# Kernel tuning notes

Hardware: AMD Instinct MI355X
Metric: run time of the kernel (lower is better)

The kernel has to match this reference:

```python
import jax, jax.numpy as jnp
import numpy as np

KLD_SCALE = 10.0
COMMITMENT_COST = 0.25


def setup_inputs() -> dict:
    key = jax.random.key(0)
    k1, k2 = jax.random.split(key)
    B, N, D, K = 8192, 32, 64, 1024
    z = jax.random.normal(k1, (B, N, D), dtype=jnp.float32)
    embed_w = jax.random.normal(k2, (K, N * D), dtype=jnp.float32)
    return {"z": z, "embed_w": embed_w}


def reference(z, embed_w):
    B, N, D = z.shape
    zf = z.reshape(B, N * D)  # b (n d)
    # squared L2 distance to each codebook vector via GEMM expansion
    dist = (jnp.sum(zf * zf, axis=1, keepdims=True)
            - 2.0 * zf @ embed_w.T
            + jnp.sum(embed_w * embed_w, axis=1)[None, :])  # [B, K]
    ind = jnp.argmin(dist, axis=1)  # [B]
    z_q = embed_w[ind]  # [B, N*D] gather
    latent_loss = (COMMITMENT_COST * jnp.mean((jax.lax.stop_gradient(z_q) - zf) ** 2)
                   + jnp.mean((z_q - jax.lax.stop_gradient(zf)) ** 2))
    latent_loss = latent_loss * KLD_SCALE
    z_q = zf + jax.lax.stop_gradient(z_q - zf)  # straight-through
    return z_q, latent_loss
```

## Files before the change

### kernel.cpp

```cpp
#include <hip/hip_runtime.h>

#define NB 8192
#define NK 1024
#define ND 2048
#define DELTA 4.0f

typedef __bf16 bf16x8 __attribute__((ext_vector_type(8)));
typedef float f32x4 __attribute__((ext_vector_type(4)));

static __device__ __forceinline__ unsigned short f2bf(float f) {
    unsigned u = __float_as_uint(f);
    unsigned r = (u + 0x7fff + ((u >> 16) & 1)) >> 16;
    return (unsigned short)r;
}

static __device__ __forceinline__ void async16(const void* g, void* l) {
    __builtin_amdgcn_global_load_lds(
        (const __attribute__((address_space(1))) void*)g,
        (__attribute__((address_space(3))) void*)l, 16, 0, 0);
}

static __device__ __forceinline__ unsigned skey(float s) {
    unsigned u = __float_as_uint(s);
    return (s >= 0.f) ? (u | 0x80000000u) : ~u;
}

static __device__ __forceinline__ void conv_row(const float* __restrict__ src,
                                                unsigned short* __restrict__ dst,
                                                float* __restrict__ nrm, int l) {
    const float4* row = (const float4*)src;
    ushort4* orow = (ushort4*)dst;
    float s = 0.f;
#pragma unroll
    for (int i = 0; i < 8; ++i) {
        float4 v = row[l + 64 * i];
        s += v.x * v.x + v.y * v.y + v.z * v.z + v.w * v.w;
        ushort4 h;
        h.x = f2bf(v.x); h.y = f2bf(v.y); h.z = f2bf(v.z); h.w = f2bf(v.w);
        orow[l + 64 * i] = h;
    }
#pragma unroll
    for (int m = 32; m; m >>= 1) s += __shfl_xor(s, m, 64);
    if (l == 0) *nrm = s;
}

__global__ __launch_bounds__(256)
void prep_kernel(const float* __restrict__ z, const float* __restrict__ e,
                 unsigned short* __restrict__ zh, unsigned short* __restrict__ eh,
                 float* __restrict__ znorm, float* __restrict__ enorm) {
    const int w = threadIdx.x >> 6, l = threadIdx.x & 63;
    if (blockIdx.x < NB / 4) {
        const int b = blockIdx.x * 4 + w;
        conv_row(z + (size_t)b * ND, zh + (size_t)b * ND, znorm + b, l);
    } else {
        const int k = (blockIdx.x - NB / 4) * 4 + w;
        conv_row(e + (size_t)k * ND, eh + (size_t)k * ND, enorm + k, l);
    }
}

__global__ __launch_bounds__(256)
void coarse_gemm_kernel(const unsigned short* __restrict__ zh,
                        const unsigned short* __restrict__ eh,
                        const float* __restrict__ enorm,
                        float* __restrict__ pmin, ulonglong2* __restrict__ pmask) {
    __shared__ __align__(16) unsigned short As[128 * 64];
    __shared__ __align__(16) unsigned short Bs[128 * 64];
    __shared__ float rmin[128][2];
    __shared__ unsigned long long rmask[128][2];

    const int t = threadIdx.x;
    const int w = t >> 6, l = t & 63;
    const int wr = w & 1, wc = w >> 1;
    const int rowBase = blockIdx.x * 128;
    const int colBase = blockIdx.y * 128;

    f32x4 acc[4][4];
#pragma unroll
    for (int m = 0; m < 4; ++m)
#pragma unroll
        for (int n = 0; n < 4; ++n) acc[m][n] = (f32x4)(0.0f);

    const int r0  = t >> 3;
    const int csw = (t & 7) ^ (r0 & 7);
    const size_t zsrc = (size_t)(rowBase + r0) * ND + csw * 8;
    const size_t esrc = (size_t)(colBase + r0) * ND + csw * 8;

    for (int k0 = 0; k0 < ND; k0 += 64) {
#pragma unroll
        for (int i = 0; i < 4; ++i) {
            async16(zh + zsrc + (size_t)i * 32 * ND + k0, &As[i * 2048 + w * 512]);
            async16(eh + esrc + (size_t)i * 32 * ND + k0, &Bs[i * 2048 + w * 512]);
        }
        __syncthreads();
#pragma unroll
        for (int kk = 0; kk < 2; ++kk) {
            bf16x8 af[4], bfr[4];
#pragma unroll
            for (int m = 0; m < 4; ++m) {
                int r = wr * 64 + m * 16 + (l & 15);
                int ch = ((l >> 4) + kk * 4) ^ (l & 7);
                af[m] = *(const bf16x8*)&As[r * 64 + ch * 8];
            }
#pragma unroll
            for (int n = 0; n < 4; ++n) {
                int r = wc * 64 + n * 16 + (l & 15);
                int ch = ((l >> 4) + kk * 4) ^ (l & 7);
                bfr[n] = *(const bf16x8*)&Bs[r * 64 + ch * 8];
            }
#pragma unroll
            for (int m = 0; m < 4; ++m)
#pragma unroll
                for (int n = 0; n < 4; ++n)
                    acc[m][n] = __builtin_amdgcn_mfma_f32_16x16x32_bf16(af[m], bfr[n], acc[m][n], 0, 0, 0);
        }
        __syncthreads();
    }

    float en[4];
#pragma unroll
    for (int n = 0; n < 4; ++n)
        en[n] = enorm[colBase + wc * 64 + n * 16 + (l & 15)];
    const int g = l >> 4;

#pragma unroll
    for (int m = 0; m < 4; ++m) {
#pragma unroll
        for (int j = 0; j < 4; ++j) {
            float mn = 3.0e38f;
#pragma unroll
            for (int n = 0; n < 4; ++n)
                mn = fminf(mn, en[n] - 2.0f * acc[m][n][j]);
#pragma unroll
            for (int d = 1; d < 16; d <<= 1) mn = fminf(mn, __shfl_xor(mn, d, 64));
            if ((l & 15) == 0) rmin[wr * 64 + m * 16 + g * 4 + j][wc] = mn;
        }
    }
    __syncthreads();

#pragma unroll
    for (int m = 0; m < 4; ++m) {
#pragma unroll
        for (int j = 0; j < 4; ++j) {
            int rl = wr * 64 + m * 16 + g * 4 + j;
            float thr = fminf(rmin[rl][0], rmin[rl][1]) + DELTA;
            unsigned long long seg = 0;
#pragma unroll
            for (int n = 0; n < 4; ++n) {
                unsigned long long bal = __ballot((en[n] - 2.0f * acc[m][n][j]) <= thr);
                seg |= ((bal >> (16 * g)) & 0xFFFFull) << (n * 16);
            }
            if ((l & 15) == 0) rmask[rl][wc] = seg;
        }
    }
    __syncthreads();
    if (t < 128) {
        size_t idx = (size_t)(rowBase + t) * 8 + blockIdx.y;
        pmin[idx] = fminf(rmin[t][0], rmin[t][1]);
        ulonglong2 mk; mk.x = rmask[t][0]; mk.y = rmask[t][1];
        pmask[idx] = mk;
    }
}

__global__ __launch_bounds__(256)
void tail_kernel(const float* __restrict__ pmin, const ulonglong2* __restrict__ pmask,
                 const float* __restrict__ z, const float* __restrict__ e,
                 const float* __restrict__ enorm, const float* __restrict__ znorm,
                 float* __restrict__ out, float* __restrict__ loss) {
    __shared__ float red[4];
    const int w = threadIdx.x >> 6, l = threadIdx.x & 63;
    const int b = blockIdx.x * 4 + w;

    float v = pmin[(size_t)b * 8 + (l & 7)];
#pragma unroll
    for (int d = 1; d < 8; d <<= 1) v = fminf(v, __shfl_xor(v, d, 64));
    const float thr = v + DELTA;

    unsigned long long mlo = 0, mhi = 0;
    int cnt = 0, kc = -1;
    if (l < 8) {
        float pc = pmin[(size_t)b * 8 + l];
        if (pc <= thr) {
            ulonglong2 mk = pmask[(size_t)b * 8 + l];
            mlo = mk.x; mhi = mk.y;
            cnt = __popcll(mlo) + __popcll(mhi);
            if (cnt) kc = l * 128 + (mlo ? (__ffsll((long long)mlo) - 1)
                                         : 64 + (__ffsll((long long)mhi) - 1));
        }
    }
    int tot = cnt;
#pragma unroll
    for (int d = 1; d < 8; d <<= 1) {
        tot += __shfl_xor(tot, d, 64);
        kc = max(kc, __shfl_xor(kc, d, 64));
    }
    tot = __shfl(tot, 0, 64);
    kc  = __shfl(kc, 0, 64);

    int bestk;
    float srow;
    if (tot == 1) {
        bestk = kc;
        srow  = v;
    } else {
        float bestv = 3.0e38f; bestk = 0x7fffffff;
        const float4* z4 = (const float4*)(z + (size_t)b * ND);
        for (int c = 0; c < 8; ++c) {
            unsigned long long lo = __shfl(mlo, c, 64);
            unsigned long long hi = __shfl(mhi, c, 64);
            while (lo | hi) {
                int k;
                if (lo) { int bit = __ffsll((long long)lo) - 1; lo &= lo - 1; k = c * 128 + bit; }
                else    { int bit = __ffsll((long long)hi) - 1; hi &= hi - 1; k = c * 128 + 64 + bit; }
                const float4* e4 = (const float4*)(e + (size_t)k * ND);
                float dot = 0.f;
#pragma unroll
                for (int q = 0; q < 8; ++q) {
                    float4 a = z4[l + 64 * q], bb = e4[l + 64 * q];
                    dot += a.x * bb.x + a.y * bb.y + a.z * bb.z + a.w * bb.w;
                }
#pragma unroll
                for (int d2 = 32; d2; d2 >>= 1) dot += __shfl_xor(dot, d2, 64);
                float s = enorm[k] - 2.0f * dot;
                if (s < bestv) { bestv = s; bestk = k; }
            }
        }
        srow = bestv;
    }

    const float4* q4 = (const float4*)(e + (size_t)bestk * ND);
    float4* o4 = (float4*)(out + (size_t)b * ND);
#pragma unroll
    for (int i = 0; i < 8; ++i) o4[l + 64 * i] = q4[l + 64 * i];

    if (l == 0) red[w] = znorm[b] + srow;
    __syncthreads();
    if (threadIdx.x == 0) {
        float s = (red[0] + red[1]) + (red[2] + red[3]);
        atomicAdd(loss, s * (12.5f / 16777216.0f));
    }
}

#define BK 16
#define LDS_STRIDE 20

__global__ void enorm_kernel(const float* __restrict__ e, float* __restrict__ enorm) {
    const int k = blockIdx.x;
    const int lane = threadIdx.x;
    const float4* row = (const float4*)(e + (size_t)k * ND);
    float s = 0.f;
#pragma unroll
    for (int i = 0; i < 8; ++i) {
        float4 v = row[lane + 64 * i];
        s += v.x * v.x + v.y * v.y + v.z * v.z + v.w * v.w;
    }
#pragma unroll
    for (int m = 32; m; m >>= 1) s += __shfl_xor(s, m, 64);
    if (lane == 0) enorm[k] = s;
}

__global__ __launch_bounds__(256, 2)
void argmin_kernel(const float* __restrict__ z, const float* __restrict__ e,
                   const float* __restrict__ enorm,
                   float* __restrict__ pminv, int* __restrict__ pmini) {
    __shared__ float zs[128 * LDS_STRIDE];
    __shared__ float es[128 * LDS_STRIDE];
    const int t  = threadIdx.x;
    const int tx = t & 31;
    const int ty = t >> 5;
    const int rowBase = blockIdx.x * 128;
    const int colBase = blockIdx.y * 128;

    float acc[16][4];
#pragma unroll
    for (int i = 0; i < 16; ++i)
#pragma unroll
        for (int j = 0; j < 4; ++j) acc[i][j] = 0.f;

    const int srow = t >> 2;
    const int sc4  = t & 3;

    for (int k0 = 0; k0 < ND; k0 += BK) {
#pragma unroll
        for (int q = 0; q < 2; ++q) {
            int r = srow + 64 * q;
            float4 vz = *(const float4*)(z + (size_t)(rowBase + r) * ND + k0 + sc4 * 4);
            *(float4*)(zs + r * LDS_STRIDE + sc4 * 4) = vz;
            float4 ve = *(const float4*)(e + (size_t)(colBase + r) * ND + k0 + sc4 * 4);
            *(float4*)(es + r * LDS_STRIDE + sc4 * 4) = ve;
        }
        __syncthreads();
#pragma unroll
        for (int g = 0; g < BK / 4; ++g) {
            float4 ef[4];
#pragma unroll
            for (int j = 0; j < 4; ++j)
                ef[j] = *(const float4*)(es + (tx + 32 * j) * LDS_STRIDE + g * 4);
#pragma unroll
            for (int i = 0; i < 16; ++i) {
                float4 zf = *(const float4*)(zs + (ty + 8 * i) * LDS_STRIDE + g * 4);
#pragma unroll
                for (int j = 0; j < 4; ++j) {
                    acc[i][j] += zf.x * ef[j].x;
                    acc[i][j] += zf.y * ef[j].y;
                    acc[i][j] += zf.z * ef[j].z;
                    acc[i][j] += zf.w * ef[j].w;
                }
            }
        }
        __syncthreads();
    }
#pragma unroll
    for (int i = 0; i < 16; ++i) {
        float bv = 3.0e38f; int bi = 0x7fffffff;
#pragma unroll
        for (int j = 0; j < 4; ++j) {
            int cg = colBase + tx + 32 * j;
            float s = enorm[cg] - 2.0f * acc[i][j];
            if (s < bv) { bv = s; bi = cg; }
        }
#pragma unroll
        for (int m = 16; m; m >>= 1) {
            float ov = __shfl_xor(bv, m, 64);
            int   oi = __shfl_xor(bi, m, 64);
            if (ov < bv || (ov == bv && oi < bi)) { bv = ov; bi = oi; }
        }
        if (tx == 0) {
            int r = rowBase + ty + 8 * i;
            pminv[(size_t)r * 8 + blockIdx.y] = bv;
            pmini[(size_t)r * 8 + blockIdx.y] = bi;
        }
    }
}

__global__ void final_argmin_kernel(const float* __restrict__ pminv,
                                    const int* __restrict__ pmini,
                                    int* __restrict__ ind) {
    int b = blockIdx.x * 256 + threadIdx.x;
    if (b >= NB) return;
    float bv = pminv[(size_t)b * 8];
    int   bi = pmini[(size_t)b * 8];
#pragma unroll
    for (int c = 1; c < 8; ++c) {
        float v  = pminv[(size_t)b * 8 + c];
        int   i2 = pmini[(size_t)b * 8 + c];
        if (v < bv || (v == bv && i2 < bi)) { bv = v; bi = i2; }
    }
    ind[b] = bi;
}

__global__ __launch_bounds__(256)
void gather_loss_kernel(const float* __restrict__ z, const float* __restrict__ e,
                        const int* __restrict__ ind, float* __restrict__ out,
                        float* __restrict__ loss) {
    const int NT4 = NB * ND / 4;
    float accm = 0.f;
    for (int f = blockIdx.x * blockDim.x + threadIdx.x; f < NT4;
         f += gridDim.x * blockDim.x) {
        int b  = f >> 9;
        int k4 = f & 511;
        const float4 q  = *(const float4*)(e + (size_t)ind[b] * ND + (size_t)k4 * 4);
        const float4 zz = *(const float4*)(z + (size_t)f * 4);
        *(float4*)(out + (size_t)f * 4) = q;
        float dx = q.x - zz.x, dy = q.y - zz.y, dz = q.z - zz.z, dw = q.w - zz.w;
        accm += dx * dx + dy * dy + dz * dz + dw * dw;
    }
#pragma unroll
    for (int m = 32; m; m >>= 1) accm += __shfl_xor(accm, m, 64);
    __shared__ float red[4];
    int lane = threadIdx.x & 63, w = threadIdx.x >> 6;
    if (lane == 0) red[w] = accm;
    __syncthreads();
    if (threadIdx.x == 0) {
        float s = (red[0] + red[1]) + (red[2] + red[3]);
        atomicAdd(loss, s * (12.5f / 16777216.0f));
    }
}

extern "C" void kernel_launch(void* const* d_in, const int* in_sizes, int n_in,
                              void* d_out, int out_size, void* d_ws, size_t ws_size,
                              hipStream_t stream) {
    const float* z = (const float*)d_in[0];
    const float* e = (const float*)d_in[1];
    float* out  = (float*)d_out;
    float* loss = out + (size_t)NB * ND;
    char* W = (char*)d_ws;

    const size_t OFF_ZH    = 0;
    const size_t OFF_EH    = 33554432;
    const size_t OFF_PMIN  = 37748736;
    const size_t OFF_PMASK = 38010880;
    const size_t OFF_EN    = 39059456;
    const size_t OFF_ZN    = 39063552;
    const size_t NEED_FAST = 39096320 + 4096;

    hipMemsetAsync(loss, 0, sizeof(float), stream);

    if (ws_size >= NEED_FAST) {
        unsigned short* zh = (unsigned short*)(W + OFF_ZH);
        unsigned short* eh = (unsigned short*)(W + OFF_EH);
        float* pmin        = (float*)(W + OFF_PMIN);
        ulonglong2* pmask  = (ulonglong2*)(W + OFF_PMASK);
        float* enorm       = (float*)(W + OFF_EN);
        float* znorm       = (float*)(W + OFF_ZN);

        hipLaunchKernelGGL(prep_kernel, dim3(NB / 4 + NK / 4), dim3(256), 0, stream,
                           z, e, zh, eh, znorm, enorm);
        hipLaunchKernelGGL(coarse_gemm_kernel, dim3(NB / 128, NK / 128), dim3(256), 0, stream,
                           zh, eh, enorm, pmin, pmask);
        hipLaunchKernelGGL(tail_kernel, dim3(NB / 4), dim3(256), 0, stream,
                           pmin, pmask, z, e, enorm, znorm, out, loss);
    } else {
        float* enorm = (float*)W;
        float* pminv = (float*)(W + 4096);
        int*   pmini = (int*)(W + 4096 + 262144);
        int*   ind   = (int*)(W + 4096 + 524288);

        hipLaunchKernelGGL(enorm_kernel, dim3(NK), dim3(64), 0, stream, e, enorm);
        hipLaunchKernelGGL(argmin_kernel, dim3(NB / 128, NK / 128), dim3(256), 0, stream,
                           z, e, enorm, pminv, pmini);
        hipLaunchKernelGGL(final_argmin_kernel, dim3(NB / 256), dim3(256), 0, stream,
                           pminv, pmini, ind);
        hipLaunchKernelGGL(gather_loss_kernel, dim3(2048), dim3(256), 0, stream,
                           z, e, ind, out, loss);
    }
}
```

Baseline: 98.47 us.

## Use 128x256 GEMM tiles with triple-buffered async pipeline and split tail kernels

The coarse GEMM grows to 512-thread blocks covering 128x256 output tiles. Operand loads are triple-buffered through LDS with explicit vmcnt waits and raw barriers, and MFMA issue is bracketed with setprio so prefetch overlaps compute. The tail kernel is split into a resolve kernel that writes packed (score, index) keys, a single-block loss reduction that replaces the memset and atomics, and a grid-stride gather kernel. The intent is to cut redundant operand loads and hide memory latency, at the cost of two extra kernel launches and a serial single-block loss pass.

```diff
diff --git a/kernel.cpp b/kernel.cpp
--- a/kernel.cpp
+++ b/kernel.cpp
@@ -7,6 +7,10 @@
 
 typedef __bf16 bf16x8 __attribute__((ext_vector_type(8)));
 typedef float f32x4 __attribute__((ext_vector_type(4)));
+
+#define FENCE asm volatile("" ::: "memory")
+#define WAIT_VM6 asm volatile("s_waitcnt vmcnt(6)" ::: "memory")
+#define WAIT_VM0 asm volatile("s_waitcnt vmcnt(0)" ::: "memory")
 
 static __device__ __forceinline__ unsigned short f2bf(float f) {
     unsigned u = __float_as_uint(f);
@@ -58,21 +62,21 @@
     }
 }
 
-__global__ __launch_bounds__(256)
-void coarse_gemm_kernel(const unsigned short* __restrict__ zh,
-                        const unsigned short* __restrict__ eh,
-                        const float* __restrict__ enorm,
-                        float* __restrict__ pmin, ulonglong2* __restrict__ pmask) {
-    __shared__ __align__(16) unsigned short As[128 * 64];
-    __shared__ __align__(16) unsigned short Bs[128 * 64];
-    __shared__ float rmin[128][2];
-    __shared__ unsigned long long rmask[128][2];
+__global__ __launch_bounds__(512, 1)
+void gemm8_kernel(const unsigned short* __restrict__ zh,
+                  const unsigned short* __restrict__ eh,
+                  const float* __restrict__ enorm,
+                  float* __restrict__ pmin, ulonglong2* __restrict__ pmask) {
+    __shared__ __align__(16) unsigned short S[3 * 24576];
+    __shared__ float rmin[128][4];
+    __shared__ unsigned long long rmask[128][4];
 
     const int t = threadIdx.x;
     const int w = t >> 6, l = t & 63;
-    const int wr = w & 1, wc = w >> 1;
+    const int wr = w >> 2, wc = w & 3;
+    const int lr = l & 15, lg = l >> 4, lx = l & 7;
     const int rowBase = blockIdx.x * 128;
-    const int colBase = blockIdx.y * 128;
+    const int colBase = blockIdx.y * 256;
 
     f32x4 acc[4][4];
 #pragma unroll
@@ -80,47 +84,86 @@
 #pragma unroll
         for (int n = 0; n < 4; ++n) acc[m][n] = (f32x4)(0.0f);
 
-    const int r0  = t >> 3;
-    const int csw = (t & 7) ^ (r0 & 7);
-    const size_t zsrc = (size_t)(rowBase + r0) * ND + csw * 8;
-    const size_t esrc = (size_t)(colBase + r0) * ND + csw * 8;
-
-    for (int k0 = 0; k0 < ND; k0 += 64) {
-#pragma unroll
-        for (int i = 0; i < 4; ++i) {
-            async16(zh + zsrc + (size_t)i * 32 * ND + k0, &As[i * 2048 + w * 512]);
-            async16(eh + esrc + (size_t)i * 32 * ND + k0, &Bs[i * 2048 + w * 512]);
-        }
-        __syncthreads();
-#pragma unroll
-        for (int kk = 0; kk < 2; ++kk) {
-            bf16x8 af[4], bfr[4];
-#pragma unroll
-            for (int m = 0; m < 4; ++m) {
-                int r = wr * 64 + m * 16 + (l & 15);
-                int ch = ((l >> 4) + kk * 4) ^ (l & 7);
-                af[m] = *(const bf16x8*)&As[r * 64 + ch * 8];
-            }
-#pragma unroll
-            for (int n = 0; n < 4; ++n) {
-                int r = wc * 64 + n * 16 + (l & 15);
-                int ch = ((l >> 4) + kk * 4) ^ (l & 7);
-                bfr[n] = *(const bf16x8*)&Bs[r * 64 + ch * 8];
-            }
-#pragma unroll
-            for (int m = 0; m < 4; ++m)
-#pragma unroll
-                for (int n = 0; n < 4; ++n)
-                    acc[m][n] = __builtin_amdgcn_mfma_f32_16x16x32_bf16(af[m], bfr[n], acc[m][n], 0, 0, 0);
-        }
-        __syncthreads();
-    }
+    const int r = t >> 3;
+    const int csw = (t & 7) ^ (r & 7);
+    const unsigned short* zsrc = zh + (size_t)(rowBase + r) * ND + csw * 8;
+    const unsigned short* esrc = eh + (size_t)(colBase + r) * ND + csw * 8;
+    const int wofs = w * 512;
+
+#define STAGE_H0(K0, SL) do { \
+        async16(zsrc + (K0),           &S[(SL) * 24576 +         wofs]); \
+        async16(zsrc + 64 * ND + (K0), &S[(SL) * 24576 +  4096 + wofs]); \
+        async16(esrc + (K0),           &S[(SL) * 24576 +  8192 + wofs]); } while (0)
+#define STAGE_H1(K0, SL) do { \
+        async16(esrc +  64 * ND + (K0), &S[(SL) * 24576 + 12288 + wofs]); \
+        async16(esrc + 128 * ND + (K0), &S[(SL) * 24576 + 16384 + wofs]); \
+        async16(esrc + 192 * ND + (K0), &S[(SL) * 24576 + 20480 + wofs]); } while (0)
+
+    STAGE_H0(0, 0);  STAGE_H1(0, 0);
+    STAGE_H0(64, 1); STAGE_H1(64, 1);
+    WAIT_VM6; FENCE; __builtin_amdgcn_s_barrier(); FENCE;
+
+    int scur = 0;
+    for (int tau = 0; tau < 32; ++tau) {
+        const unsigned short* SA = &S[scur * 24576];
+        const unsigned short* SB = SA + 8192;
+        const int spre = (scur == 0) ? 2 : scur - 1;
+        const int kpre = (tau + 2) * 64;
+
+        if (tau < 30) STAGE_H0(kpre, spre);
+        bf16x8 bfr[4][2], af[2][2];
+#pragma unroll
+        for (int n = 0; n < 4; ++n)
+#pragma unroll
+            for (int kk = 0; kk < 2; ++kk)
+                bfr[n][kk] = *(const bf16x8*)&SB[(wc * 64 + n * 16 + lr) * 64
+                                                 + (((lg + kk * 4) ^ lx) * 8)];
+#pragma unroll
+        for (int mm = 0; mm < 2; ++mm)
+#pragma unroll
+            for (int kk = 0; kk < 2; ++kk)
+                af[mm][kk] = *(const bf16x8*)&SA[(wr * 64 + mm * 16 + lr) * 64
+                                                 + (((lg + kk * 4) ^ lx) * 8)];
+        __builtin_amdgcn_s_setprio(1);
+#pragma unroll
+        for (int mm = 0; mm < 2; ++mm)
+#pragma unroll
+            for (int n = 0; n < 4; ++n)
+#pragma unroll
+                for (int kk = 0; kk < 2; ++kk)
+                    acc[mm][n] = __builtin_amdgcn_mfma_f32_16x16x32_bf16(
+                        af[mm][kk], bfr[n][kk], acc[mm][n], 0, 0, 0);
+        __builtin_amdgcn_s_setprio(0);
+
+        if (tau < 30) STAGE_H1(kpre, spre);
+#pragma unroll
+        for (int mm = 0; mm < 2; ++mm)
+#pragma unroll
+            for (int kk = 0; kk < 2; ++kk)
+                af[mm][kk] = *(const bf16x8*)&SA[(wr * 64 + (mm + 2) * 16 + lr) * 64
+                                                 + (((lg + kk * 4) ^ lx) * 8)];
+        __builtin_amdgcn_s_setprio(1);
+#pragma unroll
+        for (int mm = 0; mm < 2; ++mm)
+#pragma unroll
+            for (int n = 0; n < 4; ++n)
+#pragma unroll
+                for (int kk = 0; kk < 2; ++kk)
+                    acc[mm + 2][n] = __builtin_amdgcn_mfma_f32_16x16x32_bf16(
+                        af[mm][kk], bfr[n][kk], acc[mm + 2][n], 0, 0, 0);
+        __builtin_amdgcn_s_setprio(0);
+
+        if (tau < 30) { WAIT_VM6; } else { WAIT_VM0; }
+        FENCE; __builtin_amdgcn_s_barrier(); FENCE;
+        scur = (scur == 2) ? 0 : scur + 1;
+    }
+#undef STAGE_H0
+#undef STAGE_H1
 
     float en[4];
 #pragma unroll
     for (int n = 0; n < 4; ++n)
-        en[n] = enorm[colBase + wc * 64 + n * 16 + (l & 15)];
-    const int g = l >> 4;
+        en[n] = enorm[colBase + wc * 64 + n * 16 + lr];
 
 #pragma unroll
     for (int m = 0; m < 4; ++m) {
@@ -132,7 +175,7 @@
                 mn = fminf(mn, en[n] - 2.0f * acc[m][n][j]);
 #pragma unroll
             for (int d = 1; d < 16; d <<= 1) mn = fminf(mn, __shfl_xor(mn, d, 64));
-            if ((l & 15) == 0) rmin[wr * 64 + m * 16 + g * 4 + j][wc] = mn;
+            if (lr == 0) rmin[wr * 64 + m * 16 + lg * 4 + j][wc] = mn;
         }
     }
     __syncthreads();
@@ -141,32 +184,36 @@
     for (int m = 0; m < 4; ++m) {
 #pragma unroll
         for (int j = 0; j < 4; ++j) {
-            int rl = wr * 64 + m * 16 + g * 4 + j;
-            float thr = fminf(rmin[rl][0], rmin[rl][1]) + DELTA;
+            int rl = wr * 64 + m * 16 + lg * 4 + j;
+            float thr = fminf(fminf(rmin[rl][0], rmin[rl][1]),
+                              fminf(rmin[rl][2], rmin[rl][3])) + DELTA;
             unsigned long long seg = 0;
 #pragma unroll
             for (int n = 0; n < 4; ++n) {
                 unsigned long long bal = __ballot((en[n] - 2.0f * acc[m][n][j]) <= thr);
-                seg |= ((bal >> (16 * g)) & 0xFFFFull) << (n * 16);
+                seg |= ((bal >> (16 * lg)) & 0xFFFFull) << (n * 16);
             }
-            if ((l & 15) == 0) rmask[rl][wc] = seg;
+            if (lr == 0) rmask[rl][wc] = seg;
         }
     }
     __syncthreads();
+
     if (t < 128) {
-        size_t idx = (size_t)(rowBase + t) * 8 + blockIdx.y;
-        pmin[idx] = fminf(rmin[t][0], rmin[t][1]);
-        ulonglong2 mk; mk.x = rmask[t][0]; mk.y = rmask[t][1];
-        pmask[idx] = mk;
+        float m4 = fminf(fminf(rmin[t][0], rmin[t][1]), fminf(rmin[t][2], rmin[t][3]));
+        size_t idx = (size_t)(rowBase + t) * 8 + (size_t)blockIdx.y * 2;
+        pmin[idx] = m4;
+        ulonglong2 mk0; mk0.x = rmask[t][0]; mk0.y = rmask[t][1];
+        pmask[idx] = mk0;
+        pmin[idx + 1] = m4;
+        ulonglong2 mk1; mk1.x = rmask[t][2]; mk1.y = rmask[t][3];
+        pmask[idx + 1] = mk1;
     }
 }
 
 __global__ __launch_bounds__(256)
-void tail_kernel(const float* __restrict__ pmin, const ulonglong2* __restrict__ pmask,
-                 const float* __restrict__ z, const float* __restrict__ e,
-                 const float* __restrict__ enorm, const float* __restrict__ znorm,
-                 float* __restrict__ out, float* __restrict__ loss) {
-    __shared__ float red[4];
+void resolve2_kernel(const float* __restrict__ pmin, const ulonglong2* __restrict__ pmask,
+                     const float* __restrict__ z, const float* __restrict__ e,
+                     const float* __restrict__ enorm, unsigned long long* __restrict__ best) {
     const int w = threadIdx.x >> 6, l = threadIdx.x & 63;
     const int b = blockIdx.x * 4 + w;
 
@@ -196,47 +243,65 @@
     tot = __shfl(tot, 0, 64);
     kc  = __shfl(kc, 0, 64);
 
-    int bestk;
-    float srow;
     if (tot == 1) {
-        bestk = kc;
-        srow  = v;
-    } else {
-        float bestv = 3.0e38f; bestk = 0x7fffffff;
-        const float4* z4 = (const float4*)(z + (size_t)b * ND);
-        for (int c = 0; c < 8; ++c) {
-            unsigned long long lo = __shfl(mlo, c, 64);
-            unsigned long long hi = __shfl(mhi, c, 64);
-            while (lo | hi) {
-                int k;
-                if (lo) { int bit = __ffsll((long long)lo) - 1; lo &= lo - 1; k = c * 128 + bit; }
-                else    { int bit = __ffsll((long long)hi) - 1; hi &= hi - 1; k = c * 128 + 64 + bit; }
-                const float4* e4 = (const float4*)(e + (size_t)k * ND);
-                float dot = 0.f;
-#pragma unroll
-                for (int q = 0; q < 8; ++q) {
-                    float4 a = z4[l + 64 * q], bb = e4[l + 64 * q];
-                    dot += a.x * bb.x + a.y * bb.y + a.z * bb.z + a.w * bb.w;
-                }
-#pragma unroll
-                for (int d2 = 32; d2; d2 >>= 1) dot += __shfl_xor(dot, d2, 64);
-                float s = enorm[k] - 2.0f * dot;
-                if (s < bestv) { bestv = s; bestk = k; }
+        if (l == 0) best[b] = ((unsigned long long)skey(v) << 32) | (unsigned)kc;
+        return;
+    }
+
+    float bestv = 3.0e38f; int bestk = 0x7fffffff;
+    const float4* z4 = (const float4*)(z + (size_t)b * ND);
+    for (int c = 0; c < 8; ++c) {
+        unsigned long long lo = __shfl(mlo, c, 64);
+        unsigned long long hi = __shfl(mhi, c, 64);
+        while (lo | hi) {
+            int k;
+            if (lo) { int bit = __ffsll((long long)lo) - 1; lo &= lo - 1; k = c * 128 + bit; }
+            else    { int bit = __ffsll((long long)hi) - 1; hi &= hi - 1; k = c * 128 + 64 + bit; }
+            const float4* e4 = (const float4*)(e + (size_t)k * ND);
+            float dot = 0.f;
+#pragma unroll
+            for (int q = 0; q < 8; ++q) {
+                float4 a = z4[l + 64 * q], bb = e4[l + 64 * q];
+                dot += a.x * bb.x + a.y * bb.y + a.z * bb.z + a.w * bb.w;
             }
-        }
-        srow = bestv;
-    }
-
-    const float4* q4 = (const float4*)(e + (size_t)bestk * ND);
-    float4* o4 = (float4*)(out + (size_t)b * ND);
-#pragma unroll
-    for (int i = 0; i < 8; ++i) o4[l + 64 * i] = q4[l + 64 * i];
-
-    if (l == 0) red[w] = znorm[b] + srow;
+#pragma unroll
+            for (int d2 = 32; d2; d2 >>= 1) dot += __shfl_xor(dot, d2, 64);
+            float s = enorm[k] - 2.0f * dot;
+            if (s < bestv) { bestv = s; bestk = k; }
+        }
+    }
+    if (l == 0) best[b] = ((unsigned long long)skey(bestv) << 32) | (unsigned)bestk;
+}
+
+__global__ __launch_bounds__(256)
+void loss1_kernel(const unsigned long long* __restrict__ best,
+                  const float* __restrict__ znorm, float* __restrict__ loss) {
+    float s = 0.f;
+    for (int b = threadIdx.x; b < NB; b += 256) {
+        unsigned key = (unsigned)(best[b] >> 32);
+        unsigned ub = (key & 0x80000000u) ? (key ^ 0x80000000u) : ~key;
+        s += znorm[b] + __uint_as_float(ub);
+    }
+#pragma unroll
+    for (int m = 32; m; m >>= 1) s += __shfl_xor(s, m, 64);
+    __shared__ float red[4];
+    int lane = threadIdx.x & 63, w = threadIdx.x >> 6;
+    if (lane == 0) red[w] = s;
     __syncthreads();
-    if (threadIdx.x == 0) {
-        float s = (red[0] + red[1]) + (red[2] + red[3]);
-        atomicAdd(loss, s * (12.5f / 16777216.0f));
+    if (threadIdx.x == 0)
+        loss[0] = ((red[0] + red[1]) + (red[2] + red[3])) * (12.5f / 16777216.0f);
+}
+
+__global__ __launch_bounds__(256)
+void gather_kernel(const float* __restrict__ e, const unsigned long long* __restrict__ best,
+                   float* __restrict__ out) {
+    const int NT4 = NB * ND / 4;
+    for (int f = blockIdx.x * blockDim.x + threadIdx.x; f < NT4;
+         f += gridDim.x * blockDim.x) {
+        int b  = f >> 9;
+        int k4 = f & 511;
+        int k = (int)(best[b] & 1023ull);
+        ((float4*)out)[f] = *(const float4*)(e + (size_t)k * ND + (size_t)k4 * 4);
     }
 }
 
@@ -391,9 +456,8 @@
     const size_t OFF_PMASK = 38010880;
     const size_t OFF_EN    = 39059456;
     const size_t OFF_ZN    = 39063552;
-    const size_t NEED_FAST = 39096320 + 4096;
-
-    hipMemsetAsync(loss, 0, sizeof(float), stream);
+    const size_t OFF_BEST  = 39096320;
+    const size_t NEED_FAST = 39161856 + 4096;
 
     if (ws_size >= NEED_FAST) {
         unsigned short* zh = (unsigned short*)(W + OFF_ZH);
@@ -402,19 +466,24 @@
         ulonglong2* pmask  = (ulonglong2*)(W + OFF_PMASK);
         float* enorm       = (float*)(W + OFF_EN);
         float* znorm       = (float*)(W + OFF_ZN);
+        unsigned long long* best = (unsigned long long*)(W + OFF_BEST);
 
         hipLaunchKernelGGL(prep_kernel, dim3(NB / 4 + NK / 4), dim3(256), 0, stream,
                            z, e, zh, eh, znorm, enorm);
-        hipLaunchKernelGGL(coarse_gemm_kernel, dim3(NB / 128, NK / 128), dim3(256), 0, stream,
+        hipLaunchKernelGGL(gemm8_kernel, dim3(NB / 128, NK / 256), dim3(512), 0, stream,
                            zh, eh, enorm, pmin, pmask);
-        hipLaunchKernelGGL(tail_kernel, dim3(NB / 4), dim3(256), 0, stream,
-                           pmin, pmask, z, e, enorm, znorm, out, loss);
+        hipLaunchKernelGGL(resolve2_kernel, dim3(NB / 4), dim3(256), 0, stream,
+                           pmin, pmask, z, e, enorm, best);
+        hipLaunchKernelGGL(loss1_kernel, dim3(1), dim3(256), 0, stream,
+                           best, znorm, loss);
+        hipLaunchKernelGGL(gather_kernel, dim3(2048), dim3(256), 0, stream, e, best, out);
     } else {
         float* enorm = (float*)W;
         float* pminv = (float*)(W + 4096);
         int*   pmini = (int*)(W + 4096 + 262144);
         int*   ind   = (int*)(W + 4096 + 524288);
 
+        hipMemsetAsync(loss, 0, sizeof(float), stream);
         hipLaunchKernelGGL(enorm_kernel, dim3(NK), dim3(64), 0, stream, e, enorm);
         hipLaunchKernelGGL(argmin_kernel, dim3(NB / 128, NK / 128), dim3(256), 0, stream,
                            z, e, enorm, pminv, pmini);
```

Measured after the change: 104.4 us. 6.0% more time.

## Split tail into resolve and grid-stride gather kernels with deterministic loss reduction

Applied to the files above, without the earlier changes.

The fused tail kernel is split in two. The first kernel only resolves the argmin per row and packs the sortable key and index into a 64-bit value. The second kernel does a flat grid-stride gather of codebook rows into the output, and one dedicated block reduces the loss without atomics, which also removes the memset on the fast path. The intent is to decouple the irregular candidate-resolution work from the bandwidth-bound copy so the copy runs at full occupancy. The cost is an extra kernel launch and a round trip through the best array.

```diff
diff --git a/kernel.cpp b/kernel.cpp
--- a/kernel.cpp
+++ b/kernel.cpp
@@ -162,11 +162,9 @@
 }
 
 __global__ __launch_bounds__(256)
-void tail_kernel(const float* __restrict__ pmin, const ulonglong2* __restrict__ pmask,
-                 const float* __restrict__ z, const float* __restrict__ e,
-                 const float* __restrict__ enorm, const float* __restrict__ znorm,
-                 float* __restrict__ out, float* __restrict__ loss) {
-    __shared__ float red[4];
+void resolve2_kernel(const float* __restrict__ pmin, const ulonglong2* __restrict__ pmask,
+                     const float* __restrict__ z, const float* __restrict__ e,
+                     const float* __restrict__ enorm, unsigned long long* __restrict__ best) {
     const int w = threadIdx.x >> 6, l = threadIdx.x & 63;
     const int b = blockIdx.x * 4 + w;
 
@@ -196,47 +194,65 @@
     tot = __shfl(tot, 0, 64);
     kc  = __shfl(kc, 0, 64);
 
-    int bestk;
-    float srow;
     if (tot == 1) {
-        bestk = kc;
-        srow  = v;
-    } else {
-        float bestv = 3.0e38f; bestk = 0x7fffffff;
-        const float4* z4 = (const float4*)(z + (size_t)b * ND);
-        for (int c = 0; c < 8; ++c) {
-            unsigned long long lo = __shfl(mlo, c, 64);
-            unsigned long long hi = __shfl(mhi, c, 64);
-            while (lo | hi) {
-                int k;
-                if (lo) { int bit = __ffsll((long long)lo) - 1; lo &= lo - 1; k = c * 128 + bit; }
-                else    { int bit = __ffsll((long long)hi) - 1; hi &= hi - 1; k = c * 128 + 64 + bit; }
-                const float4* e4 = (const float4*)(e + (size_t)k * ND);
-                float dot = 0.f;
-#pragma unroll
-                for (int q = 0; q < 8; ++q) {
-                    float4 a = z4[l + 64 * q], bb = e4[l + 64 * q];
-                    dot += a.x * bb.x + a.y * bb.y + a.z * bb.z + a.w * bb.w;
-                }
-#pragma unroll
-                for (int d2 = 32; d2; d2 >>= 1) dot += __shfl_xor(dot, d2, 64);
-                float s = enorm[k] - 2.0f * dot;
-                if (s < bestv) { bestv = s; bestk = k; }
+        if (l == 0) best[b] = ((unsigned long long)skey(v) << 32) | (unsigned)kc;
+        return;
+    }
+
+    float bestv = 3.0e38f; int bestk = 0x7fffffff;
+    const float4* z4 = (const float4*)(z + (size_t)b * ND);
+    for (int c = 0; c < 8; ++c) {
+        unsigned long long lo = __shfl(mlo, c, 64);
+        unsigned long long hi = __shfl(mhi, c, 64);
+        while (lo | hi) {
+            int k;
+            if (lo) { int bit = __ffsll((long long)lo) - 1; lo &= lo - 1; k = c * 128 + bit; }
+            else    { int bit = __ffsll((long long)hi) - 1; hi &= hi - 1; k = c * 128 + 64 + bit; }
+            const float4* e4 = (const float4*)(e + (size_t)k * ND);
+            float dot = 0.f;
+#pragma unroll
+            for (int q = 0; q < 8; ++q) {
+                float4 a = z4[l + 64 * q], bb = e4[l + 64 * q];
+                dot += a.x * bb.x + a.y * bb.y + a.z * bb.z + a.w * bb.w;
             }
-        }
-        srow = bestv;
-    }
-
-    const float4* q4 = (const float4*)(e + (size_t)bestk * ND);
-    float4* o4 = (float4*)(out + (size_t)b * ND);
-#pragma unroll
-    for (int i = 0; i < 8; ++i) o4[l + 64 * i] = q4[l + 64 * i];
-
-    if (l == 0) red[w] = znorm[b] + srow;
-    __syncthreads();
-    if (threadIdx.x == 0) {
-        float s = (red[0] + red[1]) + (red[2] + red[3]);
-        atomicAdd(loss, s * (12.5f / 16777216.0f));
+#pragma unroll
+            for (int d2 = 32; d2; d2 >>= 1) dot += __shfl_xor(dot, d2, 64);
+            float s = enorm[k] - 2.0f * dot;
+            if (s < bestv) { bestv = s; bestk = k; }
+        }
+    }
+    if (l == 0) best[b] = ((unsigned long long)skey(bestv) << 32) | (unsigned)bestk;
+}
+
+__global__ __launch_bounds__(256)
+void gather_loss2_kernel(const float* __restrict__ e,
+                         const unsigned long long* __restrict__ best,
+                         const float* __restrict__ znorm,
+                         float* __restrict__ out, float* __restrict__ loss) {
+    if (blockIdx.x == gridDim.x - 1) {
+        float s = 0.f;
+        for (int b = threadIdx.x; b < NB; b += 256) {
+            unsigned key = (unsigned)(best[b] >> 32);
+            unsigned ub = (key & 0x80000000u) ? (key ^ 0x80000000u) : ~key;
+            s += znorm[b] + __uint_as_float(ub);
+        }
+#pragma unroll
+        for (int m = 32; m; m >>= 1) s += __shfl_xor(s, m, 64);
+        __shared__ float red[4];
+        int lane = threadIdx.x & 63, w = threadIdx.x >> 6;
+        if (lane == 0) red[w] = s;
+        __syncthreads();
+        if (threadIdx.x == 0)
+            loss[0] = ((red[0] + red[1]) + (red[2] + red[3])) * (12.5f / 16777216.0f);
+        return;
+    }
+    const int NT4 = NB * ND / 4;
+    const int nstream = (gridDim.x - 1) * blockDim.x;
+    for (int f = blockIdx.x * blockDim.x + threadIdx.x; f < NT4; f += nstream) {
+        int b  = f >> 9;
+        int k4 = f & 511;
+        int k = (int)(best[b] & 1023ull);
+        ((float4*)out)[f] = *(const float4*)(e + (size_t)k * ND + (size_t)k4 * 4);
     }
 }
 
@@ -391,9 +407,8 @@
     const size_t OFF_PMASK = 38010880;
     const size_t OFF_EN    = 39059456;
     const size_t OFF_ZN    = 39063552;
-    const size_t NEED_FAST = 39096320 + 4096;
-
-    hipMemsetAsync(loss, 0, sizeof(float), stream);
+    const size_t OFF_BEST  = 39096320;
+    const size_t NEED_FAST = 39161856 + 4096;
 
     if (ws_size >= NEED_FAST) {
         unsigned short* zh = (unsigned short*)(W + OFF_ZH);
@@ -402,19 +417,23 @@
         ulonglong2* pmask  = (ulonglong2*)(W + OFF_PMASK);
         float* enorm       = (float*)(W + OFF_EN);
         float* znorm       = (float*)(W + OFF_ZN);
+        unsigned long long* best = (unsigned long long*)(W + OFF_BEST);
 
         hipLaunchKernelGGL(prep_kernel, dim3(NB / 4 + NK / 4), dim3(256), 0, stream,
                            z, e, zh, eh, znorm, enorm);
         hipLaunchKernelGGL(coarse_gemm_kernel, dim3(NB / 128, NK / 128), dim3(256), 0, stream,
                            zh, eh, enorm, pmin, pmask);
-        hipLaunchKernelGGL(tail_kernel, dim3(NB / 4), dim3(256), 0, stream,
-                           pmin, pmask, z, e, enorm, znorm, out, loss);
+        hipLaunchKernelGGL(resolve2_kernel, dim3(NB / 4), dim3(256), 0, stream,
+                           pmin, pmask, z, e, enorm, best);
+        hipLaunchKernelGGL(gather_loss2_kernel, dim3(2049), dim3(256), 0, stream,
+                           e, best, znorm, out, loss);
     } else {
         float* enorm = (float*)W;
         float* pminv = (float*)(W + 4096);
         int*   pmini = (int*)(W + 4096 + 262144);
         int*   ind   = (int*)(W + 4096 + 524288);
 
+        hipMemsetAsync(loss, 0, sizeof(float), stream);
         hipLaunchKernelGGL(enorm_kernel, dim3(NK), dim3(64), 0, stream, e, enorm);
         hipLaunchKernelGGL(argmin_kernel, dim3(NB / 128, NK / 128), dim3(256), 0, stream,
                            z, e, enorm, pminv, pmini);
```

Result: faster. 88.96 us, median of 2 (-9.7%).
